# Performance work log

Measured on AMD Instinct MI355X. Metric: run time of the kernel, lower is better.

Reference implementation:

```python
import jax, jax.numpy as jnp
import numpy as np

B, S, H = 2, 2048, 768
NH = 12
HD = H // NH  # 64

def setup_inputs() -> dict:
    key = jax.random.key(0)
    ks = jax.random.split(key, 7)
    scale = 0.02
    return {
        "hidden_states": jax.random.normal(ks[0], (B, S, H), dtype=jnp.float32),
        "Wq": jax.random.normal(ks[1], (H, H), dtype=jnp.float32) * scale,
        "bq": jax.random.normal(ks[2], (H,), dtype=jnp.float32) * scale,
        "Wk": jax.random.normal(ks[3], (H, H), dtype=jnp.float32) * scale,
        "bk": jax.random.normal(ks[4], (H,), dtype=jnp.float32) * scale,
        "Wv": jax.random.normal(ks[5], (H, H), dtype=jnp.float32) * scale,
        "bv": jax.random.normal(ks[6], (H,), dtype=jnp.float32) * scale,
    }

def _split_heads(x):
    # [B, S, H] -> [B, NH, S, HD]
    b, s, _ = x.shape
    return x.reshape(b, s, NH, HD).transpose(0, 2, 1, 3)

def reference(hidden_states, Wq, bq, Wk, bk, Wv, bv):
    q = _split_heads(hidden_states @ Wq + bq)  # [B, NH, S, HD]
    k = _split_heads(hidden_states @ Wk + bk)
    v = _split_heads(hidden_states @ Wv + bv)
    scores = jnp.einsum('bhqd,bhkd->bhqk', q, k) / jnp.sqrt(jnp.float32(HD))
    probs = jax.nn.softmax(scores, axis=-1)  # dropout prob = 0 (eval)
    ctx = jnp.einsum('bhqk,bhkd->bhqd', probs, v)  # [B, NH, S, HD]
    ctx = ctx.transpose(0, 2, 1, 3).reshape(hidden_states.shape[0], hidden_states.shape[1], NH * HD)
    return ctx
```

## Files before the change

### kernel.cpp

```cpp
#include <hip/hip_runtime.h>
#include <math.h>

#define B_  2
#define S_  2048
#define H_  768
#define NH_ 12
#define HD_ 64
#define M_  (B_ * S_)
#define BH_ (B_ * NH_)

typedef __attribute__((ext_vector_type(8))) short bf16x8;
typedef __attribute__((ext_vector_type(4))) short bf16x4;
typedef __attribute__((ext_vector_type(4))) float f32x4;

static __device__ __forceinline__ short f2bf(float x) {
  unsigned u = __builtin_bit_cast(unsigned, x);
  u += 0x7FFFu + ((u >> 16) & 1u);
  return (short)(u >> 16);
}

#define MFMA16(a, b, c) __builtin_amdgcn_mfma_f32_16x16x32_bf16((a), (b), (c), 0, 0, 0)

__global__ __launch_bounds__(256) void xprep_kernel(const float* __restrict__ X,
                                                    short* __restrict__ Xb) {
  const int i = (blockIdx.x * 256 + threadIdx.x) * 8;
  const float4 a = *(const float4*)&X[i];
  const float4 b = *(const float4*)&X[i + 4];
  short tmp[8] = {f2bf(a.x), f2bf(a.y), f2bf(a.z), f2bf(a.w),
                  f2bf(b.x), f2bf(b.y), f2bf(b.z), f2bf(b.w)};
  *(bf16x8*)&Xb[i] = *(const bf16x8*)tmp;
}

__global__ __launch_bounds__(256) void wprep_kernel(
    const float* __restrict__ Wq, const float* __restrict__ Wk,
    const float* __restrict__ Wv, short* __restrict__ Wt) {
  const int mat = blockIdx.z;
  const float* W = (mat == 0) ? Wq : (mat == 1 ? Wk : Wv);
  const int bk = blockIdx.x * 64, bn = blockIdx.y * 64;
  __shared__ float T[64][68];
  const int t = threadIdx.x;
  {
    const int n = t & 63, kq = t >> 6;
#pragma unroll
    for (int u = 0; u < 16; ++u) {
      const int k = kq * 16 + u;
      T[k][n] = W[(size_t)(bk + k) * H_ + bn + n];
    }
  }
  __syncthreads();
  {
    const int n = t >> 2, c0 = (t & 3) * 16;
    short tmp[16];
#pragma unroll
    for (int j = 0; j < 16; ++j) tmp[j] = f2bf(T[c0 + j][n]);
    short* dst = Wt + ((size_t)mat * H_ + bn + n) * H_ + bk + c0;
    *(bf16x8*)dst = *(const bf16x8*)tmp;
    *(bf16x8*)(dst + 8) = *(const bf16x8*)(tmp + 8);
  }
}

__global__ __launch_bounds__(256) void qkv_gemm_kernel(
    const short* __restrict__ Xb, const short* __restrict__ Wt,
    const float* __restrict__ bq, const float* __restrict__ bk,
    const float* __restrict__ bv, short* __restrict__ QKV) {
  const int mat = blockIdx.z;
  const float* bias = (mat == 0) ? bq : (mat == 1 ? bk : bv);
  const float qscale = (mat == 0) ? 0.125f : 1.0f;
  const short* Wm = Wt + (size_t)mat * H_ * H_;
  short* out = QKV + (size_t)mat * M_ * HD_ * NH_;

  __shared__ short Xs[128][40];
  __shared__ short Ws[64][40];

  const int t = threadIdx.x;
  const int w = t >> 6, l = t & 63, c = l & 15, g = l >> 4;
  const int wm = w >> 1, wn = w & 1;
  const int bm = blockIdx.x * 128, bn = blockIdx.y * 64;

  const f32x4 fz = {0.f, 0.f, 0.f, 0.f};
  f32x4 acc[4][2];
#pragma unroll
  for (int i = 0; i < 4; ++i) { acc[i][0] = fz; acc[i][1] = fz; }

  for (int k0 = 0; k0 < H_; k0 += 32) {
    {
#pragma unroll
      for (int u = 0; u < 2; ++u) {
        const int i = u * 256 + t;
        const int row = i >> 2, kc = (i & 3) * 8;
        *(bf16x8*)&Xs[row][kc] =
            *(const bf16x8*)&Xb[(size_t)(bm + row) * H_ + k0 + kc];
      }
      const int n = t >> 2, kc = (t & 3) * 8;
      *(bf16x8*)&Ws[n][kc] = *(const bf16x8*)&Wm[(size_t)(bn + n) * H_ + k0 + kc];
    }
    __syncthreads();
    bf16x8 af[4], bfr[2];
#pragma unroll
    for (int mt = 0; mt < 4; ++mt)
      af[mt] = *(const bf16x8*)&Xs[wm * 64 + mt * 16 + c][g * 8];
#pragma unroll
    for (int nt = 0; nt < 2; ++nt)
      bfr[nt] = *(const bf16x8*)&Ws[wn * 32 + nt * 16 + c][g * 8];
#pragma unroll
    for (int mt = 0; mt < 4; ++mt)
#pragma unroll
      for (int nt = 0; nt < 2; ++nt)
        acc[mt][nt] = MFMA16(af[mt], bfr[nt], acc[mt][nt]);
    __syncthreads();
  }

  const int h = blockIdx.y;
#pragma unroll
  for (int nt = 0; nt < 2; ++nt) {
    const int col = wn * 32 + nt * 16 + c;
    const float bsc = bias[bn + col] * qscale;
#pragma unroll
    for (int mt = 0; mt < 4; ++mt) {
#pragma unroll
      for (int r = 0; r < 4; ++r) {
        const int row = bm + wm * 64 + mt * 16 + g * 4 + r;
        const int bb = row >> 11, ss = row & (S_ - 1);
        out[((size_t)(bb * NH_ + h) * S_ + ss) * HD_ + col] =
            f2bf(acc[mt][nt][r] * qscale + bsc);
      }
    }
  }
}

__global__ __launch_bounds__(256) void vtrans_kernel(const short* __restrict__ V,
                                                     short* __restrict__ Vt) {
  const int bh = blockIdx.y, s0 = blockIdx.x * 64;
  __shared__ short T[64][72];
  const int t = threadIdx.x;
  {
    const short* src = V + ((size_t)bh * S_ + s0) * HD_;
#pragma unroll
    for (int u = 0; u < 2; ++u) {
      const int i = u * 256 + t;
      *(bf16x8*)&T[i >> 3][(i & 7) * 8] = *(const bf16x8*)&src[i * 8];
    }
  }
  __syncthreads();
  {
    const int d = t >> 2, sc = (t & 3) * 16;
    short tmp[16];
#pragma unroll
    for (int j = 0; j < 16; ++j) tmp[j] = T[sc + j][d];
    short* dst = Vt + ((size_t)bh * HD_ + d) * S_ + s0 + sc;
    *(bf16x8*)dst = *(const bf16x8*)tmp;
    *(bf16x8*)(dst + 8) = *(const bf16x8*)(tmp + 8);
  }
}

__global__ __launch_bounds__(256) void attn_kernel(const short* __restrict__ Q,
                                                   const short* __restrict__ K,
                                                   const short* __restrict__ Vt,
                                                   float* __restrict__ out) {
  __shared__ short Qs[64][72], Ks[64][72], Vs[64][72];
  __shared__ short Ps[4][16][72];

  const int t = threadIdx.x;
  const int w = t >> 6, l = t & 63, c = l & 15, g = l >> 4;
  const int qt = blockIdx.x, bh = blockIdx.y;
  const size_t base = (size_t)bh * S_ * HD_;

  {
    const short* src = Q + base + (size_t)qt * 64 * HD_;
#pragma unroll
    for (int u = 0; u < 2; ++u) {
      const int i = u * 256 + t;
      *(bf16x8*)&Qs[i >> 3][(i & 7) * 8] = *(const bf16x8*)&src[i * 8];
    }
  }

  const f32x4 fz = {0.f, 0.f, 0.f, 0.f};
  f32x4 ctx[4];
  float m_i[4], l_i[4];
#pragma unroll
  for (int r = 0; r < 4; ++r) { m_i[r] = -INFINITY; l_i[r] = 0.f; ctx[r] = fz; }

  for (int kt = 0; kt < S_ / 64; ++kt) {
    {
      const short* ksrc = K + base + (size_t)kt * 64 * HD_;
#pragma unroll
      for (int u = 0; u < 2; ++u) {
        const int i = u * 256 + t;
        *(bf16x8*)&Ks[i >> 3][(i & 7) * 8] = *(const bf16x8*)&ksrc[i * 8];
      }
      const short* vsrc = Vt + (size_t)bh * HD_ * S_ + kt * 64;
      const int d = t >> 2;
#pragma unroll
      for (int u = 0; u < 2; ++u) {
        const int ch = ((t & 3) + u * 4) * 8;
        *(bf16x8*)&Vs[d][ch] = *(const bf16x8*)&vsrc[(size_t)d * S_ + ch];
      }
    }
    __syncthreads();

    f32x4 sc[4] = {fz, fz, fz, fz};
    bf16x8 qa[2];
#pragma unroll
    for (int ks = 0; ks < 2; ++ks)
      qa[ks] = *(const bf16x8*)&Qs[w * 16 + c][ks * 32 + g * 8];
#pragma unroll
    for (int nt = 0; nt < 4; ++nt)
#pragma unroll
      for (int ks = 0; ks < 2; ++ks) {
        const bf16x8 kb = *(const bf16x8*)&Ks[nt * 16 + c][ks * 32 + g * 8];
        sc[nt] = MFMA16(qa[ks], kb, sc[nt]);
      }

#pragma unroll
    for (int r = 0; r < 4; ++r) {
      float mx = fmaxf(fmaxf(sc[0][r], sc[1][r]), fmaxf(sc[2][r], sc[3][r]));
#pragma unroll
      for (int off = 1; off <= 8; off <<= 1) mx = fmaxf(mx, __shfl_xor(mx, off));
      const float mnew = fmaxf(m_i[r], mx);
      const float rs = __expf(m_i[r] - mnew);
      const float p0 = __expf(sc[0][r] - mnew), p1 = __expf(sc[1][r] - mnew);
      const float p2 = __expf(sc[2][r] - mnew), p3 = __expf(sc[3][r] - mnew);
      float ps = p0 + p1 + p2 + p3;
#pragma unroll
      for (int off = 1; off <= 8; off <<= 1) ps += __shfl_xor(ps, off);
      l_i[r] = l_i[r] * rs + ps;
      m_i[r] = mnew;
#pragma unroll
      for (int dt = 0; dt < 4; ++dt) ctx[dt][r] *= rs;
      Ps[w][g * 4 + r][c]      = f2bf(p0);
      Ps[w][g * 4 + r][16 + c] = f2bf(p1);
      Ps[w][g * 4 + r][32 + c] = f2bf(p2);
      Ps[w][g * 4 + r][48 + c] = f2bf(p3);
    }

    bf16x8 pa[2];
#pragma unroll
    for (int kb = 0; kb < 2; ++kb)
      pa[kb] = *(const bf16x8*)&Ps[w][c][kb * 32 + g * 8];
#pragma unroll
    for (int dt = 0; dt < 4; ++dt)
#pragma unroll
      for (int kb = 0; kb < 2; ++kb) {
        const bf16x8 vb = *(const bf16x8*)&Vs[dt * 16 + c][kb * 32 + g * 8];
        ctx[dt] = MFMA16(pa[kb], vb, ctx[dt]);
      }
    __syncthreads();
  }

  const int bb = bh / NH_, hh = bh % NH_;
#pragma unroll
  for (int r = 0; r < 4; ++r) {
    const float inv = 1.f / l_i[r];
    const int s = qt * 64 + w * 16 + g * 4 + r;
#pragma unroll
    for (int dt = 0; dt < 4; ++dt)
      out[((size_t)bb * S_ + s) * H_ + hh * HD_ + dt * 16 + c] = ctx[dt][r] * inv;
  }
}

extern "C" void kernel_launch(void* const* d_in, const int* in_sizes, int n_in,
                              void* d_out, int out_size, void* d_ws, size_t ws_size,
                              hipStream_t stream) {
  const float* X  = (const float*)d_in[0];
  const float* Wq = (const float*)d_in[1];
  const float* bq = (const float*)d_in[2];
  const float* Wk = (const float*)d_in[3];
  const float* bk = (const float*)d_in[4];
  const float* Wv = (const float*)d_in[5];
  const float* bv = (const float*)d_in[6];
  float* out = (float*)d_out;

  short* ws  = (short*)d_ws;
  short* QKV = ws;
  short* Vt  = ws + (size_t)3 * M_ * H_;
  short* Wt  = ws + (size_t)4 * M_ * H_;
  short* Xb  = Wt + (size_t)3 * H_ * H_;
  const short* V = QKV + (size_t)2 * M_ * H_;

  xprep_kernel<<<dim3((M_ * H_) / (256 * 8)), 256, 0, stream>>>(X, Xb);
  wprep_kernel<<<dim3(12, 12, 3), 256, 0, stream>>>(Wq, Wk, Wv, Wt);
  qkv_gemm_kernel<<<dim3(M_ / 128, H_ / 64, 3), 256, 0, stream>>>(Xb, Wt, bq, bk, bv, QKV);
  vtrans_kernel<<<dim3(S_ / 64, BH_), 256, 0, stream>>>(V, Vt);
  attn_kernel<<<dim3(S_ / 64, BH_), 256, 0, stream>>>(QKV, QKV + (size_t)M_ * H_, Vt, out);
}
```

Baseline: 221.9 us.

## Prefetch next tiles into registers in QKV GEMM and attention, widen GEMM N tile

The QKV GEMM now uses a 128x128 output tile with a 4x4 MFMA accumulator per wave. It prefetches the next K-slice into registers while computing the current one from LDS. The attention kernel does the same double-staging for K/V tiles, keeps Q fragments in registers instead of LDS, and folds log2(e) into the Q scale so it can use exp2f. The online softmax also skips rescaling when the row max does not grow. This trades more registers and a second barrier per iteration for hiding global load latency.

Measured after the change: 207.5 us. -6.5%, faster.

```diff
diff --git a/kernel.cpp b/kernel.cpp
--- a/kernel.cpp
+++ b/kernel.cpp
@@ -8,6 +8,7 @@
 #define HD_ 64
 #define M_  (B_ * S_)
 #define BH_ (B_ * NH_)
+#define LOG2E_ 1.44269504088896f
 
 typedef __attribute__((ext_vector_type(8))) short bf16x8;
 typedef __attribute__((ext_vector_type(4))) short bf16x4;
@@ -65,64 +66,87 @@
     const float* __restrict__ bv, short* __restrict__ QKV) {
   const int mat = blockIdx.z;
   const float* bias = (mat == 0) ? bq : (mat == 1 ? bk : bv);
-  const float qscale = (mat == 0) ? 0.125f : 1.0f;
+  const float qsc = (mat == 0) ? 0.125f * LOG2E_ : 1.0f;
   const short* Wm = Wt + (size_t)mat * H_ * H_;
-  short* out = QKV + (size_t)mat * M_ * HD_ * NH_;
-
-  __shared__ short Xs[128][40];
-  __shared__ short Ws[64][40];
+  short* out = QKV + (size_t)mat * M_ * H_;
+
+  __shared__ short Xs[128][72];
+  __shared__ short Ws2[128][72];
 
   const int t = threadIdx.x;
   const int w = t >> 6, l = t & 63, c = l & 15, g = l >> 4;
   const int wm = w >> 1, wn = w & 1;
-  const int bm = blockIdx.x * 128, bn = blockIdx.y * 64;
+  const int bm = blockIdx.x * 128, bn = blockIdx.y * 128;
 
   const f32x4 fz = {0.f, 0.f, 0.f, 0.f};
-  f32x4 acc[4][2];
-#pragma unroll
-  for (int i = 0; i < 4; ++i) { acc[i][0] = fz; acc[i][1] = fz; }
-
-  for (int k0 = 0; k0 < H_; k0 += 32) {
-    {
+  f32x4 acc[4][4];
+#pragma unroll
+  for (int i = 0; i < 4; ++i)
+#pragma unroll
+    for (int j = 0; j < 4; ++j) acc[i][j] = fz;
+
+  bf16x8 xr[2], wr[2];
+#pragma unroll
+  for (int u = 0; u < 2; ++u) {
+    const int i = u * 256 + t;
+    xr[u] = *(const bf16x8*)&Xb[(size_t)(bm + (i >> 2)) * H_ + (i & 3) * 8];
+    wr[u] = *(const bf16x8*)&Wm[(size_t)(bn + (i >> 2)) * H_ + (i & 3) * 8];
+  }
+#pragma unroll
+  for (int u = 0; u < 2; ++u) {
+    const int i = u * 256 + t;
+    *(bf16x8*)&Xs[i >> 2][(i & 3) * 8] = xr[u];
+    *(bf16x8*)&Ws2[i >> 2][(i & 3) * 8] = wr[u];
+  }
+  __syncthreads();
+
+  for (int ks = 0; ks < H_ / 32; ++ks) {
+    if (ks < H_ / 32 - 1) {
+      const int k0 = (ks + 1) * 32;
 #pragma unroll
       for (int u = 0; u < 2; ++u) {
         const int i = u * 256 + t;
-        const int row = i >> 2, kc = (i & 3) * 8;
-        *(bf16x8*)&Xs[row][kc] =
-            *(const bf16x8*)&Xb[(size_t)(bm + row) * H_ + k0 + kc];
-      }
-      const int n = t >> 2, kc = (t & 3) * 8;
-      *(bf16x8*)&Ws[n][kc] = *(const bf16x8*)&Wm[(size_t)(bn + n) * H_ + k0 + kc];
-    }
-    __syncthreads();
-    bf16x8 af[4], bfr[2];
+        xr[u] = *(const bf16x8*)&Xb[(size_t)(bm + (i >> 2)) * H_ + k0 + (i & 3) * 8];
+        wr[u] = *(const bf16x8*)&Wm[(size_t)(bn + (i >> 2)) * H_ + k0 + (i & 3) * 8];
+      }
+    }
+    bf16x8 af[4], bfr[4];
 #pragma unroll
     for (int mt = 0; mt < 4; ++mt)
       af[mt] = *(const bf16x8*)&Xs[wm * 64 + mt * 16 + c][g * 8];
 #pragma unroll
-    for (int nt = 0; nt < 2; ++nt)
-      bfr[nt] = *(const bf16x8*)&Ws[wn * 32 + nt * 16 + c][g * 8];
+    for (int nt = 0; nt < 4; ++nt)
+      bfr[nt] = *(const bf16x8*)&Ws2[wn * 64 + nt * 16 + c][g * 8];
 #pragma unroll
     for (int mt = 0; mt < 4; ++mt)
 #pragma unroll
-      for (int nt = 0; nt < 2; ++nt)
+      for (int nt = 0; nt < 4; ++nt)
         acc[mt][nt] = MFMA16(af[mt], bfr[nt], acc[mt][nt]);
     __syncthreads();
-  }
-
-  const int h = blockIdx.y;
-#pragma unroll
-  for (int nt = 0; nt < 2; ++nt) {
-    const int col = wn * 32 + nt * 16 + c;
-    const float bsc = bias[bn + col] * qscale;
+    if (ks < H_ / 32 - 1) {
+#pragma unroll
+      for (int u = 0; u < 2; ++u) {
+        const int i = u * 256 + t;
+        *(bf16x8*)&Xs[i >> 2][(i & 3) * 8] = xr[u];
+        *(bf16x8*)&Ws2[i >> 2][(i & 3) * 8] = wr[u];
+      }
+      __syncthreads();
+    }
+  }
+
+#pragma unroll
+  for (int nt = 0; nt < 4; ++nt) {
+    const int col = bn + wn * 64 + nt * 16 + c;
+    const int h = col >> 6, d = col & 63;
+    const float bsc = bias[col] * qsc;
 #pragma unroll
     for (int mt = 0; mt < 4; ++mt) {
 #pragma unroll
       for (int r = 0; r < 4; ++r) {
         const int row = bm + wm * 64 + mt * 16 + g * 4 + r;
         const int bb = row >> 11, ss = row & (S_ - 1);
-        out[((size_t)(bb * NH_ + h) * S_ + ss) * HD_ + col] =
-            f2bf(acc[mt][nt][r] * qscale + bsc);
+        out[((size_t)(bb * NH_ + h) * S_ + ss) * HD_ + d] =
+            f2bf(acc[mt][nt][r] * qsc + bsc);
       }
     }
   }
@@ -157,22 +181,34 @@
                                                    const short* __restrict__ K,
                                                    const short* __restrict__ Vt,
                                                    float* __restrict__ out) {
-  __shared__ short Qs[64][72], Ks[64][72], Vs[64][72];
+  __shared__ short Ks[64][72], Vs[64][72];
   __shared__ short Ps[4][16][72];
 
   const int t = threadIdx.x;
   const int w = t >> 6, l = t & 63, c = l & 15, g = l >> 4;
   const int qt = blockIdx.x, bh = blockIdx.y;
   const size_t base = (size_t)bh * S_ * HD_;
-
-  {
-    const short* src = Q + base + (size_t)qt * 64 * HD_;
-#pragma unroll
-    for (int u = 0; u < 2; ++u) {
-      const int i = u * 256 + t;
-      *(bf16x8*)&Qs[i >> 3][(i & 7) * 8] = *(const bf16x8*)&src[i * 8];
-    }
-  }
+  const short* ksrc = K + base;
+  const short* vsrc = Vt + (size_t)bh * HD_ * S_;
+
+  bf16x8 kr[2], vr[2];
+#pragma unroll
+  for (int u = 0; u < 2; ++u) {
+    const int i = u * 256 + t;
+    kr[u] = *(const bf16x8*)&ksrc[i * 8];
+    vr[u] = *(const bf16x8*)&vsrc[(size_t)(i >> 3) * S_ + (i & 7) * 8];
+  }
+#pragma unroll
+  for (int u = 0; u < 2; ++u) {
+    const int i = u * 256 + t;
+    *(bf16x8*)&Ks[i >> 3][(i & 7) * 8] = kr[u];
+    *(bf16x8*)&Vs[i >> 3][(i & 7) * 8] = vr[u];
+  }
+  __syncthreads();
+
+  const short* qrow = Q + base + (size_t)(qt * 64 + w * 16 + c) * HD_;
+  const bf16x8 qa0 = *(const bf16x8*)&qrow[g * 8];
+  const bf16x8 qa1 = *(const bf16x8*)&qrow[32 + g * 8];
 
   const f32x4 fz = {0.f, 0.f, 0.f, 0.f};
   f32x4 ctx[4];
@@ -181,70 +217,71 @@
   for (int r = 0; r < 4; ++r) { m_i[r] = -INFINITY; l_i[r] = 0.f; ctx[r] = fz; }
 
   for (int kt = 0; kt < S_ / 64; ++kt) {
-    {
-      const short* ksrc = K + base + (size_t)kt * 64 * HD_;
+    if (kt < S_ / 64 - 1) {
+      const short* kn = ksrc + (size_t)(kt + 1) * 64 * HD_;
 #pragma unroll
       for (int u = 0; u < 2; ++u) {
         const int i = u * 256 + t;
-        *(bf16x8*)&Ks[i >> 3][(i & 7) * 8] = *(const bf16x8*)&ksrc[i * 8];
-      }
-      const short* vsrc = Vt + (size_t)bh * HD_ * S_ + kt * 64;
-      const int d = t >> 2;
-#pragma unroll
-      for (int u = 0; u < 2; ++u) {
-        const int ch = ((t & 3) + u * 4) * 8;
-        *(bf16x8*)&Vs[d][ch] = *(const bf16x8*)&vsrc[(size_t)d * S_ + ch];
-      }
-    }
-    __syncthreads();
+        kr[u] = *(const bf16x8*)&kn[i * 8];
+        vr[u] = *(const bf16x8*)&vsrc[(size_t)(i >> 3) * S_ + (kt + 1) * 64 + (i & 7) * 8];
+      }
+    }
 
     f32x4 sc[4] = {fz, fz, fz, fz};
-    bf16x8 qa[2];
-#pragma unroll
-    for (int ks = 0; ks < 2; ++ks)
-      qa[ks] = *(const bf16x8*)&Qs[w * 16 + c][ks * 32 + g * 8];
-#pragma unroll
-    for (int nt = 0; nt < 4; ++nt)
-#pragma unroll
-      for (int ks = 0; ks < 2; ++ks) {
-        const bf16x8 kb = *(const bf16x8*)&Ks[nt * 16 + c][ks * 32 + g * 8];
-        sc[nt] = MFMA16(qa[ks], kb, sc[nt]);
-      }
+#pragma unroll
+    for (int nt = 0; nt < 4; ++nt) {
+      const bf16x8 kb0 = *(const bf16x8*)&Ks[nt * 16 + c][g * 8];
+      const bf16x8 kb1 = *(const bf16x8*)&Ks[nt * 16 + c][32 + g * 8];
+      sc[nt] = MFMA16(qa0, kb0, sc[nt]);
+      sc[nt] = MFMA16(qa1, kb1, sc[nt]);
+    }
 
 #pragma unroll
     for (int r = 0; r < 4; ++r) {
       float mx = fmaxf(fmaxf(sc[0][r], sc[1][r]), fmaxf(sc[2][r], sc[3][r]));
 #pragma unroll
       for (int off = 1; off <= 8; off <<= 1) mx = fmaxf(mx, __shfl_xor(mx, off));
-      const float mnew = fmaxf(m_i[r], mx);
-      const float rs = __expf(m_i[r] - mnew);
-      const float p0 = __expf(sc[0][r] - mnew), p1 = __expf(sc[1][r] - mnew);
-      const float p2 = __expf(sc[2][r] - mnew), p3 = __expf(sc[3][r] - mnew);
+      if (__any(mx > m_i[r])) {
+        const float mnew = fmaxf(m_i[r], mx);
+        const float rs = exp2f(m_i[r] - mnew);
+        l_i[r] *= rs;
+#pragma unroll
+        for (int dt = 0; dt < 4; ++dt) ctx[dt][r] *= rs;
+        m_i[r] = mnew;
+      }
+      const float p0 = exp2f(sc[0][r] - m_i[r]), p1 = exp2f(sc[1][r] - m_i[r]);
+      const float p2 = exp2f(sc[2][r] - m_i[r]), p3 = exp2f(sc[3][r] - m_i[r]);
       float ps = p0 + p1 + p2 + p3;
 #pragma unroll
       for (int off = 1; off <= 8; off <<= 1) ps += __shfl_xor(ps, off);
-      l_i[r] = l_i[r] * rs + ps;
-      m_i[r] = mnew;
-#pragma unroll
-      for (int dt = 0; dt < 4; ++dt) ctx[dt][r] *= rs;
+      l_i[r] += ps;
       Ps[w][g * 4 + r][c]      = f2bf(p0);
       Ps[w][g * 4 + r][16 + c] = f2bf(p1);
       Ps[w][g * 4 + r][32 + c] = f2bf(p2);
       Ps[w][g * 4 + r][48 + c] = f2bf(p3);
     }
 
-    bf16x8 pa[2];
-#pragma unroll
-    for (int kb = 0; kb < 2; ++kb)
-      pa[kb] = *(const bf16x8*)&Ps[w][c][kb * 32 + g * 8];
-#pragma unroll
-    for (int dt = 0; dt < 4; ++dt)
-#pragma unroll
-      for (int kb = 0; kb < 2; ++kb) {
-        const bf16x8 vb = *(const bf16x8*)&Vs[dt * 16 + c][kb * 32 + g * 8];
-        ctx[dt] = MFMA16(pa[kb], vb, ctx[dt]);
-      }
+    {
+      const bf16x8 pa0 = *(const bf16x8*)&Ps[w][c][g * 8];
+      const bf16x8 pa1 = *(const bf16x8*)&Ps[w][c][32 + g * 8];
+#pragma unroll
+      for (int dt = 0; dt < 4; ++dt) {
+        const bf16x8 vb0 = *(const bf16x8*)&Vs[dt * 16 + c][g * 8];
+        const bf16x8 vb1 = *(const bf16x8*)&Vs[dt * 16 + c][32 + g * 8];
+        ctx[dt] = MFMA16(pa0, vb0, ctx[dt]);
+        ctx[dt] = MFMA16(pa1, vb1, ctx[dt]);
+      }
+    }
     __syncthreads();
+    if (kt < S_ / 64 - 1) {
+#pragma unroll
+      for (int u = 0; u < 2; ++u) {
+        const int i = u * 256 + t;
+        *(bf16x8*)&Ks[i >> 3][(i & 7) * 8] = kr[u];
+        *(bf16x8*)&Vs[i >> 3][(i & 7) * 8] = vr[u];
+      }
+      __syncthreads();
+    }
   }
 
   const int bb = bh / NH_, hh = bh % NH_;
@@ -279,7 +316,7 @@
 
   xprep_kernel<<<dim3((M_ * H_) / (256 * 8)), 256, 0, stream>>>(X, Xb);
   wprep_kernel<<<dim3(12, 12, 3), 256, 0, stream>>>(Wq, Wk, Wv, Wt);
-  qkv_gemm_kernel<<<dim3(M_ / 128, H_ / 64, 3), 256, 0, stream>>>(Xb, Wt, bq, bk, bv, QKV);
+  qkv_gemm_kernel<<<dim3(M_ / 128, H_ / 128, 3), 256, 0, stream>>>(Xb, Wt, bq, bk, bv, QKV);
   vtrans_kernel<<<dim3(S_ / 64, BH_), 256, 0, stream>>>(V, Vt);
   attn_kernel<<<dim3(S_ / 64, BH_), 256, 0, stream>>>(QKV, QKV + (size_t)M_ * H_, Vt, out);
 }
```
